# Optimization experiments

Hardware: AMD Instinct MI355X
Metric: run time of the kernel (lower is better)

Reference implementation:

```python
import jax, jax.numpy as jnp
import numpy as np
import math

D_MODEL = 512
HEADS = 8
D_K = D_MODEL // HEADS
N_CODES = 2048
BETA = 0.2
# conv stack config: (in_ch, out_ch, kernel, stride)
CONV_CFG = [(105, 64, 10, 3), (64, 128, 3, 2), (128, 256, 3, 2),
            (256, 512, 3, 2), (512, 512, 2, 2), (512, 512, 2, 2)]


def setup_inputs() -> dict:
    key = jax.random.key(0)
    ks = jax.random.split(key, 32)
    inp = {"x": jax.random.normal(ks[0], (64, 105, 5500), dtype=jnp.float32)}
    # conv weights [out, in, k] (OIW layout) + biases, scaled ~ 1/sqrt(fan_in)
    for i, (cin, cout, k, s) in enumerate(CONV_CFG):
        std = 1.0 / math.sqrt(cin * k)
        inp[f"w{i+1}"] = jax.random.normal(ks[1 + 2 * i], (cout, cin, k), dtype=jnp.float32) * std
        inp[f"b{i+1}"] = jax.random.normal(ks[2 + 2 * i], (cout,), dtype=jnp.float32) * std
    # per-head Q/K/V projections stacked: [H, D, d_k]
    std = 1.0 / math.sqrt(D_MODEL)
    inp["wq"] = jax.random.normal(ks[13], (HEADS, D_MODEL, D_K), dtype=jnp.float32) * std
    inp["wk"] = jax.random.normal(ks[14], (HEADS, D_MODEL, D_K), dtype=jnp.float32) * std
    inp["wv"] = jax.random.normal(ks[15], (HEADS, D_MODEL, D_K), dtype=jnp.float32) * std
    inp["wo"] = jax.random.normal(ks[16], (D_MODEL, D_MODEL), dtype=jnp.float32) * std
    inp["bo"] = jax.random.normal(ks[17], (D_MODEL,), dtype=jnp.float32) * std
    # codebook (nn.Embedding default init ~ N(0,1))
    inp["codebook"] = jax.random.normal(ks[18], (N_CODES, D_MODEL), dtype=jnp.float32)
    return inp


def _conv_stack(x, ws, bs):
    # x: [B, C, T]; valid 1D convs with given strides
    for w, b, (_, _, _, s) in zip(ws, bs, CONV_CFG):
        x = jax.lax.conv_general_dilated(
            x, w, window_strides=(s,), padding='VALID',
            dimension_numbers=('NCH', 'OIH', 'NCH'))
        x = x + b[None, :, None]
    return x  # [B, 512, 57]


def _mha(x, wq, wk, wv, wo, bo):
    # x: [B, L, D]
    q = jnp.einsum('bld,hdk->bhlk', x, wq)
    k = jnp.einsum('bld,hdk->bhlk', x, wk)
    v = jnp.einsum('bld,hdk->bhlk', x, wv)
    scores = jnp.einsum('bhlk,bhmk->bhlm', q, k) / math.sqrt(D_K)
    attn = jax.nn.softmax(scores, axis=-1)
    out = jnp.einsum('bhlm,bhmk->bhlk', attn, v)
    B, H, L, dk = out.shape
    out = out.transpose(0, 2, 1, 3).reshape(B, L, H * dk)  # concat heads
    return out @ wo + bo


def reference(x, w1, b1, w2, b2, w3, b3, w4, b4, w5, b5, w6, b6,
              wq, wk, wv, wo, bo, codebook):
    ws = [w1, w2, w3, w4, w5, w6]
    bs = [b1, b2, b3, b4, b5, b6]
    conv_out = _conv_stack(x, ws, bs).transpose(0, 2, 1)  # [B, 57, 512]
    attn = _mha(conv_out, wq, wk, wv, wo, bo)             # [B, 57, 512]
    # squared Euclidean distances to codebook (same argmin as cdist)
    d2 = (jnp.sum(attn * attn, axis=-1, keepdims=True)    # [B, L, 1]
          - 2.0 * jnp.einsum('bld,nd->bln', attn, codebook)
          + jnp.sum(codebook * codebook, axis=-1)[None, None, :])  # [B, L, N]
    indices = jnp.argmin(d2, axis=-1)                     # [B, L]
    z_q = codebook[indices]                               # [B, L, D]
    codebook_loss = jnp.mean((z_q - jax.lax.stop_gradient(attn)) ** 2)
    commitment_loss = jnp.mean((attn - jax.lax.stop_gradient(z_q)) ** 2)
    vq_loss = codebook_loss + BETA * commitment_loss
    z_q_st = attn + jax.lax.stop_gradient(z_q - attn)
    return z_q_st, vq_loss, indices
```

## Files before the change

kernel.cpp:

```cpp
#include <hip/hip_runtime.h>
#include <hip/hip_bf16.h>
#include <math.h>

#define B_ 64
#define HB_ 32
#define L_ 57
#define D_ 512
#define H_ 8
#define DK_ 64
#define NC_ 2048

__global__ __launch_bounds__(256) void wtrans_k(const float* __restrict__ w,
                                                float* __restrict__ wT,
                                                int CINK, int COUT)
{
  int idx = blockIdx.x * 256 + threadIdx.x;
  if (idx >= CINK * COUT) return;
  int r = idx / COUT, c = idx - r * COUT;
  wT[idx] = w[(size_t)c * CINK + r];
}

__global__ __launch_bounds__(256) void wqkvprep_k(
    const float* __restrict__ wq, const float* __restrict__ wk,
    const float* __restrict__ wv, float* __restrict__ wqkvT)
{
  int idx = blockIdx.x * 256 + threadIdx.x;
  if (idx >= 786432) return;
  int set = idx >> 18;
  int h   = (idx >> 15) & 7;
  int d   = (idx >> 6) & 511;
  int kd  = idx & 63;
  const float* W = (set == 0 ? wq : (set == 1 ? wk : wv));
  float v = W[((size_t)h * 512 + d) * 64 + kd];
  wqkvT[(size_t)d * 1536 + set * 512 + h * 64 + kd] = v;
}

template<int CIN, int K, int S, int COUT, int CC>
__global__ __launch_bounds__(256) void conv1d_k(
    const float* __restrict__ x, const float* __restrict__ wT,
    const float* __restrict__ bias, float* __restrict__ y,
    int Tin, int Tout)
{
  constexpr int TT = 64;
  constexpr int SPAN = S * TT + K - S;
  __shared__ float xs[CC * SPAN];
  const int b   = blockIdx.z;
  const int cbk = blockIdx.y;
  const int t0  = blockIdx.x * TT;
  const int tid = threadIdx.x;
  const int lane_t = tid & 63;
  const int g = tid >> 6;
  const int coutBase = __builtin_amdgcn_readfirstlane(cbk * 64 + g * 16);
  const int t = t0 + lane_t;
  float acc[16];
#pragma unroll
  for (int j = 0; j < 16; ++j) acc[j] = 0.f;
  const float* xb = x + (size_t)b * CIN * Tin;
  const int col0 = t0 * S;

  for (int c0 = 0; c0 < CIN; c0 += CC) {
    __syncthreads();
    for (int e = tid; e < CC * SPAN; e += 256) {
      int cc = e / SPAN, col = e - cc * SPAN;
      int ti = col0 + col;
      xs[e] = (ti < Tin) ? xb[(size_t)(c0 + cc) * Tin + ti] : 0.f;
    }
    __syncthreads();

    const float* wchunk = wT + ((size_t)c0 * K) * COUT + coutBase;
    for (int cc = 0; cc < CC; ++cc) {
#pragma unroll
      for (int kk = 0; kk < K; ++kk) {
        const float* wrow = wchunk + (size_t)(cc * K + kk) * COUT;
        float wv[16];
#pragma unroll
        for (int j = 0; j < 16; ++j) wv[j] = wrow[j];
        float xv = xs[cc * SPAN + lane_t * S + kk];
#pragma unroll
        for (int j = 0; j < 16; ++j) acc[j] += xv * wv[j];
      }
    }
  }
  if (t < Tout) {
#pragma unroll
    for (int j = 0; j < 16; ++j) {
      int co = coutBase + j;
      y[((size_t)b * COUT + co) * Tout + t] = acc[j] + bias[co];
    }
  }
}

template<int CINC, int K, int S, int COUT, int CC, int KS>
__global__ __launch_bounds__(256) void convks_k(
    const float* __restrict__ x, const float* __restrict__ wT,
    float* __restrict__ p, int Tin, int Tout, int bStrideX, int ksStrideP)
{
  constexpr int TT = 64;
  constexpr int SPAN = S * TT + K - S;
  __shared__ float xs[CC * SPAN];
  const int b   = blockIdx.z;
  const int cbk = blockIdx.y & 7;
  const int ks  = blockIdx.y >> 3;
  const int t0  = blockIdx.x * TT;
  const int tid = threadIdx.x;
  const int lane_t = tid & 63;
  const int g = tid >> 6;
  const int coutBase = __builtin_amdgcn_readfirstlane(cbk * 64 + g * 16);
  const int t = t0 + lane_t;
  float acc[16];
#pragma unroll
  for (int j = 0; j < 16; ++j) acc[j] = 0.f;
  const float* xb = x + (size_t)b * bStrideX + (size_t)ks * CINC * Tin;
  const float* wbase = wT + ((size_t)ks * CINC * K) * COUT;
  const int col0 = t0 * S;

  for (int c0 = 0; c0 < CINC; c0 += CC) {
    __syncthreads();
    for (int e = tid; e < CC * SPAN; e += 256) {
      int cc = e / SPAN, col = e - cc * SPAN;
      int ti = col0 + col;
      xs[e] = (ti < Tin) ? xb[(size_t)(c0 + cc) * Tin + ti] : 0.f;
    }
    __syncthreads();

    const float* wchunk = wbase + ((size_t)c0 * K) * COUT + coutBase;
    for (int cc = 0; cc < CC; ++cc) {
#pragma unroll
      for (int kk = 0; kk < K; ++kk) {
        const float* wrow = wchunk + (size_t)(cc * K + kk) * COUT;
        float wv[16];
#pragma unroll
        for (int j = 0; j < 16; ++j) wv[j] = wrow[j];
        float xv = xs[cc * SPAN + lane_t * S + kk];
#pragma unroll
        for (int j = 0; j < 16; ++j) acc[j] += xv * wv[j];
      }
    }
  }
  if (t < Tout) {
#pragma unroll
    for (int j = 0; j < 16; ++j) {
      int co = coutBase + j;
      p[(size_t)ks * ksStrideP + ((size_t)b * COUT + co) * Tout + t] = acc[j];
    }
  }
}

template<int COUT, int TOUT, int KS>
__global__ __launch_bounds__(256) void redbias_k(
    const float* __restrict__ p, const float* __restrict__ bias,
    float* __restrict__ y, int ksStride, int n)
{
  int idx = blockIdx.x * 256 + threadIdx.x;
  if (idx >= n) return;
  int c = (idx / TOUT) % COUT;
  float s = p[idx];
#pragma unroll
  for (int ks = 1; ks < KS; ++ks) s += p[idx + (size_t)ks * ksStride];
  y[idx] = s + bias[c];
}

__global__ __launch_bounds__(256) void itranspose_k(const float* __restrict__ y,
                                                    float* __restrict__ yT)
{
  const int b = blockIdx.y, dt = blockIdx.x;
  __shared__ float tile[32 * 58];
  const int tid = threadIdx.x;
  const int d0 = dt * 32;
  for (int e = tid; e < L_ * 32; e += 256) {
    int l = e >> 5, dd = e & 31;
    tile[dd * 58 + l] = y[((size_t)b * L_ + l) * D_ + d0 + dd];
  }
  __syncthreads();
  for (int e = tid; e < 32 * L_; e += 256) {
    int dd = e / L_, l = e - dd * L_;
    yT[((size_t)b * D_ + d0 + dd) * L_ + l] = tile[dd * 58 + l];
  }
}

__global__ __launch_bounds__(256, 2) void qkvgemm_k(
    const float* __restrict__ c6, const float* __restrict__ wqkvT,
    float* __restrict__ q, float* __restrict__ k, float* __restrict__ v)
{
  const int ot = blockIdx.x, b = blockIdx.y;
  const int tid = threadIdx.x;
  const int w = tid >> 6, lane = tid & 63;
  const int lrow = lane >> 3, ncol = lane & 7;
  __shared__ __align__(16) float As[32 * 68];
  __shared__ __align__(16) float Bs[32 * 256];
  float acc[8][8];
#pragma unroll
  for (int li = 0; li < 8; ++li)
#pragma unroll
    for (int nj = 0; nj < 8; ++nj) acc[li][nj] = 0.f;

  const float* c6b = c6 + (size_t)b * D_ * L_;
  const int o0 = ot * 256;

  for (int d0 = 0; d0 < D_; d0 += 32) {
    __syncthreads();
#pragma unroll
    for (int i = 0; i < 8; ++i) {
      int e = tid + i * 256;
      int dd = e >> 6, l = e & 63;
      As[dd * 68 + l] = (l < L_) ? c6b[(size_t)(d0 + dd) * L_ + l] : 0.f;
    }
#pragma unroll
    for (int i = 0; i < 8; ++i) {
      int e = tid + i * 256;
      int dd = e >> 6, o4 = (e & 63) * 4;
      *reinterpret_cast<float4*>(&Bs[dd * 256 + o4]) =
          *reinterpret_cast<const float4*>(&wqkvT[(size_t)(d0 + dd) * 1536 + o0 + o4]);
    }
    __syncthreads();
#pragma unroll 4
    for (int dd = 0; dd < 32; ++dd) {
      float a8[8], b8[8];
      *reinterpret_cast<float4*>(&a8[0]) = *reinterpret_cast<const float4*>(&As[dd * 68 + lrow * 8]);
      *reinterpret_cast<float4*>(&a8[4]) = *reinterpret_cast<const float4*>(&As[dd * 68 + lrow * 8 + 4]);
      *reinterpret_cast<float4*>(&b8[0]) = *reinterpret_cast<const float4*>(&Bs[dd * 256 + w * 64 + ncol * 8]);
      *reinterpret_cast<float4*>(&b8[4]) = *reinterpret_cast<const float4*>(&Bs[dd * 256 + w * 64 + ncol * 8 + 4]);
#pragma unroll
      for (int li = 0; li < 8; ++li)
#pragma unroll
        for (int nj = 0; nj < 8; ++nj)
          acc[li][nj] += a8[li] * b8[nj];
    }
  }

  const int o3 = o0 + w * 64 + ncol * 8;
  const int set = __builtin_amdgcn_readfirstlane(o3 >> 9);
  const int h = (o3 >> 6) & 7, kd = o3 & 63;
  float* OUT = (set == 0 ? q : (set == 1 ? k : v));
  float* base = OUT + (((size_t)b * H_ + h) * L_) * DK_ + kd;
#pragma unroll
  for (int li = 0; li < 8; ++li) {
    int l = lrow * 8 + li;
    if (l < L_) {
      float* p = base + (size_t)l * DK_;
      *reinterpret_cast<float4*>(p)     = *reinterpret_cast<float4*>(&acc[li][0]);
      *reinterpret_cast<float4*>(p + 4) = *reinterpret_cast<float4*>(&acc[li][4]);
    }
  }
}

__global__ __launch_bounds__(256) void attn_k(
    const float* __restrict__ q, const float* __restrict__ k, const float* __restrict__ v,
    float* __restrict__ cat)
{
  const int bh = blockIdx.x;
  const int b = bh >> 3, h = bh & 7;
  __shared__ float qs[L_ * DK_];
  __shared__ float ks[L_ * 65];
  __shared__ float vs[L_ * DK_];
  __shared__ float ps[L_ * DK_];
  const int tid = threadIdx.x;
  const float* qb = q + (size_t)bh * L_ * DK_;
  const float* kb = k + (size_t)bh * L_ * DK_;
  const float* vb = v + (size_t)bh * L_ * DK_;
  for (int e = tid; e < L_ * DK_; e += 256) {
    qs[e] = qb[e];
    vs[e] = vb[e];
    int m = e >> 6, d = e & 63;
    ks[m * 65 + d] = kb[e];
  }
  __syncthreads();
  for (int e = tid; e < L_ * L_; e += 256) {
    int l = e / L_, m = e - (e / L_) * L_;
    float s = 0.f;
#pragma unroll
    for (int d = 0; d < DK_; ++d) s += qs[l * DK_ + d] * ks[m * 65 + d];
    ps[l * DK_ + m] = s * 0.125f;
  }
  __syncthreads();
  if (tid < L_) {
    float mx = -1e30f;
    for (int m = 0; m < L_; ++m) mx = fmaxf(mx, ps[tid * DK_ + m]);
    float sum = 0.f;
    for (int m = 0; m < L_; ++m) { float e2 = __expf(ps[tid * DK_ + m] - mx); ps[tid * DK_ + m] = e2; sum += e2; }
    float inv = 1.f / sum;
    for (int m = 0; m < L_; ++m) ps[tid * DK_ + m] *= inv;
  }
  __syncthreads();
  for (int e = tid; e < L_ * DK_; e += 256) {
    int l = e >> 6, kd = e & 63;
    float s = 0.f;
    for (int m = 0; m < L_; ++m) s += ps[l * DK_ + m] * vs[m * DK_ + kd];
    cat[((size_t)b * L_ + l) * D_ + h * DK_ + kd] = s;
  }
}

__global__ __launch_bounds__(256) void outproj_k(
    const float* __restrict__ cat, const float* __restrict__ wo,
    const float* __restrict__ bo, float* __restrict__ y)
{
  const int b = blockIdx.y, lt = blockIdx.x;
  const int l0 = lt * 16;
  __shared__ __align__(16) float cs[16 * D_];
  const int tid = threadIdx.x;
  for (int e = tid; e < 16 * D_; e += 256) {
    int l = l0 + (e >> 9);
    cs[e] = (l < L_) ? cat[((size_t)b * L_ + l) * D_ + (e & 511)] : 0.f;
  }
  __syncthreads();
  float acc0[16], acc1[16];
#pragma unroll
  for (int j = 0; j < 16; ++j) { acc0[j] = 0.f; acc1[j] = 0.f; }
  for (int d = 0; d < D_; d += 4) {
    float w00 = wo[(size_t)d * D_ + tid];
    float w01 = wo[(size_t)(d + 1) * D_ + tid];
    float w02 = wo[(size_t)(d + 2) * D_ + tid];
    float w03 = wo[(size_t)(d + 3) * D_ + tid];
    float w10 = wo[(size_t)d * D_ + tid + 256];
    float w11 = wo[(size_t)(d + 1) * D_ + tid + 256];
    float w12 = wo[(size_t)(d + 2) * D_ + tid + 256];
    float w13 = wo[(size_t)(d + 3) * D_ + tid + 256];
#pragma unroll
    for (int j = 0; j < 16; ++j) {
      const float4 c4 = *reinterpret_cast<const float4*>(&cs[j * D_ + d]);
      acc0[j] += c4.x * w00 + c4.y * w01 + c4.z * w02 + c4.w * w03;
      acc1[j] += c4.x * w10 + c4.y * w11 + c4.z * w12 + c4.w * w13;
    }
  }
#pragma unroll
  for (int j = 0; j < 16; ++j) {
    int l = l0 + j;
    if (l < L_) {
      y[((size_t)b * L_ + l) * D_ + tid] = acc0[j] + bo[tid];
      y[((size_t)b * L_ + l) * D_ + tid + 256] = acc1[j] + bo[tid + 256];
    }
  }
}

__global__ __launch_bounds__(64) void cbprep_k(const float* __restrict__ cb,
                                               float* __restrict__ cbT,
                                               float* __restrict__ cnorm)
{
  const int n = blockIdx.x, t = threadIdx.x;
  float s = 0.f;
  for (int d = t; d < D_; d += 64) {
    float vv = cb[(size_t)n * D_ + d];
    cbT[(size_t)d * NC_ + n] = vv;
    s += vv * vv;
  }
#pragma unroll
  for (int off = 32; off >= 1; off >>= 1) s += __shfl_xor(s, off);
  if (t == 0) cnorm[n] = s;
}

__global__ __launch_bounds__(256, 2) void vqgemm_k(
    const float* __restrict__ yT, const float* __restrict__ cbT,
    const float* __restrict__ cnorm, float* __restrict__ pmin, int* __restrict__ pidx)
{
  const int b = blockIdx.y, nt = blockIdx.x;
  const int tid = threadIdx.x;
  const int w = tid >> 6, lane = tid & 63;
  const int lrow = lane >> 3, ncol = lane & 7;
  __shared__ __align__(16) float As[32 * 68];
  __shared__ __align__(16) float Bs[32 * 256];
  __shared__ float redv[4][64];
  __shared__ int   redi[4][64];
  float acc[8][8];
#pragma unroll
  for (int li = 0; li < 8; ++li)
#pragma unroll
    for (int nj = 0; nj < 8; ++nj) acc[li][nj] = 0.f;

  const float* yTb = yT + (size_t)b * D_ * L_;
  const int n0 = nt * 256;
  const int nbase = n0 + w * 64 + ncol * 8;

  for (int d0 = 0; d0 < D_; d0 += 32) {
    __syncthreads();
#pragma unroll
    for (int i = 0; i < 8; ++i) {
      int e = tid + i * 256;
      int dd = e >> 6, l = e & 63;
      As[dd * 68 + l] = (l < L_) ? yTb[(size_t)(d0 + dd) * L_ + l] : 0.f;
    }
#pragma unroll
    for (int i = 0; i < 8; ++i) {
      int e = tid + i * 256;
      int dd = e >> 6, n4 = (e & 63) * 4;
      *reinterpret_cast<float4*>(&Bs[dd * 256 + n4]) =
          *reinterpret_cast<const float4*>(&cbT[(size_t)(d0 + dd) * NC_ + n0 + n4]);
    }
    __syncthreads();
#pragma unroll 4
    for (int dd = 0; dd < 32; ++dd) {
      float a8[8], b8[8];
      *reinterpret_cast<float4*>(&a8[0]) = *reinterpret_cast<const float4*>(&As[dd * 68 + lrow * 8]);
      *reinterpret_cast<float4*>(&a8[4]) = *reinterpret_cast<const float4*>(&As[dd * 68 + lrow * 8 + 4]);
      *reinterpret_cast<float4*>(&b8[0]) = *reinterpret_cast<const float4*>(&Bs[dd * 256 + w * 64 + ncol * 8]);
      *reinterpret_cast<float4*>(&b8[4]) = *reinterpret_cast<const float4*>(&Bs[dd * 256 + w * 64 + ncol * 8 + 4]);
#pragma unroll
      for (int li = 0; li < 8; ++li)
#pragma unroll
        for (int nj = 0; nj < 8; ++nj)
          acc[li][nj] += a8[li] * b8[nj];
    }
  }

  float cn[8];
  *reinterpret_cast<float4*>(&cn[0]) = *reinterpret_cast<const float4*>(&cnorm[nbase]);
  *reinterpret_cast<float4*>(&cn[4]) = *reinterpret_cast<const float4*>(&cnorm[nbase + 4]);
#pragma unroll
  for (int li = 0; li < 8; ++li) {
    float vb = cn[0] - 2.f * acc[li][0];
    int ib = nbase;
#pragma unroll
    for (int nj = 1; nj < 8; ++nj) {
      float v = cn[nj] - 2.f * acc[li][nj];
      if (v < vb) { vb = v; ib = nbase + nj; }
    }
#pragma unroll
    for (int off = 1; off <= 4; off <<= 1) {
      float vo = __shfl_xor(vb, off);
      int io = __shfl_xor(ib, off);
      if (vo < vb || (vo == vb && io < ib)) { vb = vo; ib = io; }
    }
    if (ncol == 0) { redv[w][lrow * 8 + li] = vb; redi[w][lrow * 8 + li] = ib; }
  }
  __syncthreads();
  if (tid < L_) {
    float vb = redv[0][tid]; int ib = redi[0][tid];
#pragma unroll
    for (int w2 = 1; w2 < 4; ++w2) {
      float vo = redv[w2][tid]; int io = redi[w2][tid];
      if (vo < vb || (vo == vb && io < ib)) { vb = vo; ib = io; }
    }
    pmin[((size_t)b * L_ + tid) * 8 + nt] = vb;
    pidx[((size_t)b * L_ + tid) * 8 + nt] = ib;
  }
}

__global__ __launch_bounds__(64) void vqfin_k(
    const float* __restrict__ y, const float* __restrict__ cbook,
    const float* __restrict__ pmin, const int* __restrict__ pidx,
    float* __restrict__ zq, float* __restrict__ oidx, float* __restrict__ lpart)
{
  const int bl = blockIdx.x;
  const int tid = threadIdx.x;
  __shared__ int sidx;
  if (tid == 0) {
    float vb = pmin[(size_t)bl * 8];
    int ib = pidx[(size_t)bl * 8];
    for (int ntv = 1; ntv < 8; ++ntv) {
      float vo = pmin[(size_t)bl * 8 + ntv];
      int io = pidx[(size_t)bl * 8 + ntv];
      if (vo < vb || (vo == vb && io < ib)) { vb = vo; ib = io; }
    }
    sidx = ib;
  }
  __syncthreads();
  const int idx = sidx;
  const float* crow = cbook + (size_t)idx * D_;
  const float* yrow = y + (size_t)bl * D_;
  float s = 0.f;
  for (int d = tid; d < D_; d += 64) {
    float c = crow[d];
    float df = c - yrow[d];
    zq[(size_t)bl * D_ + d] = c;
    s += df * df;
  }
#pragma unroll
  for (int off = 32; off >= 1; off >>= 1) s += __shfl_xor(s, off);
  if (tid == 0) { lpart[bl] = s; oidx[bl] = (float)idx; }
}

__global__ __launch_bounds__(256) void loss_k(const float* __restrict__ lpart,
                                              float* __restrict__ outLoss)
{
  const int tid = threadIdx.x;
  float s = 0.f;
  for (int i = tid; i < B_ * L_; i += 256) s += lpart[i];
  __shared__ float red[256];
  red[tid] = s;
  __syncthreads();
  for (int off = 128; off >= 1; off >>= 1) {
    if (tid < off) red[tid] += red[tid + off];
    __syncthreads();
  }
  if (tid == 0) outLoss[0] = red[0] * ((1.f + 0.2f) / (float)((size_t)B_ * L_ * D_));
}

extern "C" void kernel_launch(void* const* d_in, const int* in_sizes, int n_in,
                              void* d_out, int out_size, void* d_ws, size_t ws_size,
                              hipStream_t stream)
{
  const float* x  = (const float*)d_in[0];
  const float* w1 = (const float*)d_in[1];  const float* b1 = (const float*)d_in[2];
  const float* w2 = (const float*)d_in[3];  const float* b2 = (const float*)d_in[4];
  const float* w3 = (const float*)d_in[5];  const float* b3 = (const float*)d_in[6];
  const float* w4 = (const float*)d_in[7];  const float* b4 = (const float*)d_in[8];
  const float* w5 = (const float*)d_in[9];  const float* b5 = (const float*)d_in[10];
  const float* w6 = (const float*)d_in[11]; const float* b6 = (const float*)d_in[12];
  const float* wq = (const float*)d_in[13];
  const float* wk = (const float*)d_in[14];
  const float* wv = (const float*)d_in[15];
  const float* wo = (const float*)d_in[16];
  const float* bo = (const float*)d_in[17];
  const float* cbook = (const float*)d_in[18];

  float* ws = (float*)d_ws;
  float* wT1 = ws;
  float* wT2 = ws + 67200;
  float* wT3 = ws + 91776;
  float* wT4 = ws + 190080;
  float* wT5 = ws + 583296;
  float* wT6 = ws + 1107584;
  float* bufA = ws + 1632000;
  float* bufB = ws + 5382016;
  float* c6   = ws + 9132032;
  float* qb     = ws;
  float* kb     = ws + 1867776;
  float* vb     = ws + 3735552;
  float* wqkvT  = ws + 5603328;
  float* cat    = ws + 7471104;
  float* yattn  = ws + 9338880;
  float* cbT    = ws + 11206656;
  float* cnorm  = ws + 12255232;
  float* pminb  = ws + 12257280;
  int*   pidxb  = (int*)(ws + 12286464);
  float* lpart  = ws + 12315648;
  float* yT     = ws;

  float* zq      = (float*)d_out;
  float* outLoss = zq + (size_t)B_ * L_ * D_;
  float* outIdx  = outLoss + 1;

  wtrans_k<<<(1050 * 64 + 255) / 256, 256, 0, stream>>>(w1, wT1, 1050, 64);
  wtrans_k<<<( 192 * 128 + 255) / 256, 256, 0, stream>>>(w2, wT2, 192, 128);
  wtrans_k<<<( 384 * 256 + 255) / 256, 256, 0, stream>>>(w3, wT3, 384, 256);
  wtrans_k<<<( 768 * 512 + 255) / 256, 256, 0, stream>>>(w4, wT4, 768, 512);
  wtrans_k<<<(1024 * 512 + 255) / 256, 256, 0, stream>>>(w5, wT5, 1024, 512);
  wtrans_k<<<(1024 * 512 + 255) / 256, 256, 0, stream>>>(w6, wT6, 1024, 512);

  for (int h = 0; h < 2; ++h) {
    const float* xh = x + (size_t)h * HB_ * 105 * 5500;
    float* c6h = c6 + (size_t)h * HB_ * D_ * L_;
    conv1d_k<105,10,3, 64,35><<<dim3(29,1,HB_),256,0,stream>>>(xh,   wT1,b1, bufA, 5500,1831);
    conv1d_k< 64, 3,2,128,64><<<dim3(15,2,HB_),256,0,stream>>>(bufA, wT2,b2, bufB, 1831, 915);
    conv1d_k<128, 3,2,256,64><<<dim3( 8,4,HB_),256,0,stream>>>(bufB, wT3,b3, bufA,  915, 457);
    conv1d_k<256, 3,2,512,64><<<dim3( 4,8,HB_),256,0,stream>>>(bufA, wT4,b4, bufB,  457, 228);
    convks_k<256,2,2,512,64,2><<<dim3(2,16,HB_),256,0,stream>>>(
        bufB, wT5, bufA, 228, 114, 512 * 228, 1867776);
    redbias_k<512,114,2><<<(1867776 + 255) / 256, 256, 0, stream>>>(
        bufA, b5, bufB, 1867776, 1867776);
    convks_k<128,2,2,512,64,4><<<dim3(1,32,HB_),256,0,stream>>>(
        bufB, wT6, bufA, 114, 57, 512 * 114, 933888);
    redbias_k<512,57,4><<<(933888 + 255) / 256, 256, 0, stream>>>(
        bufA, b6, c6h, 933888, 933888);
  }

  wqkvprep_k<<<(786432 + 255) / 256, 256, 0, stream>>>(wq, wk, wv, wqkvT);
  qkvgemm_k<<<dim3(6, B_), 256, 0, stream>>>(c6, wqkvT, qb, kb, vb);
  cbprep_k<<<NC_, 64, 0, stream>>>(cbook, cbT, cnorm);
  attn_k<<<B_ * H_, 256, 0, stream>>>(qb, kb, vb, cat);
  outproj_k<<<dim3(4, B_), 256, 0, stream>>>(cat, wo, bo, yattn);

  itranspose_k<<<dim3(16, B_), 256, 0, stream>>>(yattn, yT);
  vqgemm_k<<<dim3(8, B_), 256, 0, stream>>>(yT, cbT, cnorm, pminb, pidxb);
  vqfin_k<<<B_ * L_, 64, 0, stream>>>(yattn, cbook, pminb, pidxb, zq, outIdx, lpart);
  loss_k<<<1, 256, 0, stream>>>(lpart, outLoss);
}
```

Before: 1.379 ms.

## Unify conv kernels with channel-interleaved LDS layout and split-K first conv

Merges the two conv kernels into one templated kernel. It stores the input tile in shared memory as [time][channel] with padding, so each thread reads two channels at once with a float2 load. The first conv layer is now split across two channel groups, with weights zero-padded to a multiple of the chunk size, and a reduction-plus-bias pass afterwards. This gives the largest layer more blocks and cuts LDS load instructions. The cost is an extra partial-sum write and read for layer 1, plus more weight-row loads held in registers at the same time.

```diff
diff --git a/kernel.cpp b/kernel.cpp
--- a/kernel.cpp
+++ b/kernel.cpp
@@ -10,14 +10,14 @@
 #define DK_ 64
 #define NC_ 2048
 
-__global__ __launch_bounds__(256) void wtrans_k(const float* __restrict__ w,
-                                                float* __restrict__ wT,
-                                                int CINK, int COUT)
+__global__ __launch_bounds__(256) void wtransp_k(const float* __restrict__ w,
+                                                 float* __restrict__ wT,
+                                                 int CINK, int CINK_PAD, int COUT)
 {
   int idx = blockIdx.x * 256 + threadIdx.x;
-  if (idx >= CINK * COUT) return;
+  if (idx >= CINK_PAD * COUT) return;
   int r = idx / COUT, c = idx - r * COUT;
-  wT[idx] = w[(size_t)c * CINK + r];
+  wT[idx] = (r < CINK) ? w[(size_t)c * CINK + r] : 0.f;
 }
 
 __global__ __launch_bounds__(256) void wqkvprep_k(
@@ -35,17 +35,21 @@
   wqkvT[(size_t)d * 1536 + set * 512 + h * 64 + kd] = v;
 }
 
-template<int CIN, int K, int S, int COUT, int CC>
-__global__ __launch_bounds__(256) void conv1d_k(
+template<int CC, int K, int S, int COUT, bool PARTIAL>
+__global__ __launch_bounds__(256) void convq_k(
     const float* __restrict__ x, const float* __restrict__ wT,
     const float* __restrict__ bias, float* __restrict__ y,
-    int Tin, int Tout)
+    int Tin, int Tout, int CINtot, int nChunks, int nCoutBlk,
+    int ksStrideP, int cinPerKs)
 {
   constexpr int TT = 64;
   constexpr int SPAN = S * TT + K - S;
-  __shared__ float xs[CC * SPAN];
+  constexpr int CCP = CC + 2;
+  __shared__ __align__(16) float xs[SPAN * CCP];
   const int b   = blockIdx.z;
-  const int cbk = blockIdx.y;
+  const int yb  = blockIdx.y;
+  const int cbk = yb % nCoutBlk;
+  const int ks  = yb / nCoutBlk;
   const int t0  = blockIdx.x * TT;
   const int tid = threadIdx.x;
   const int lane_t = tid & 63;
@@ -55,29 +59,39 @@
   float acc[16];
 #pragma unroll
   for (int j = 0; j < 16; ++j) acc[j] = 0.f;
-  const float* xb = x + (size_t)b * CIN * Tin;
+  const float* xb = x + (size_t)b * CINtot * Tin;
   const int col0 = t0 * S;
-
-  for (int c0 = 0; c0 < CIN; c0 += CC) {
+  const int cinBase = ks * cinPerKs;
+
+  for (int ch = 0; ch < nChunks; ++ch) {
+    const int cin0 = cinBase + ch * CC;
     __syncthreads();
     for (int e = tid; e < CC * SPAN; e += 256) {
       int cc = e / SPAN, col = e - cc * SPAN;
+      int gci = cin0 + cc;
       int ti = col0 + col;
-      xs[e] = (ti < Tin) ? xb[(size_t)(c0 + cc) * Tin + ti] : 0.f;
-    }
-    __syncthreads();
-
-    const float* wchunk = wT + ((size_t)c0 * K) * COUT + coutBase;
-    for (int cc = 0; cc < CC; ++cc) {
+      float v = 0.f;
+      if (ti < Tin && gci < CINtot) v = xb[(size_t)gci * Tin + ti];
+      xs[col * CCP + cc] = v;
+    }
+    __syncthreads();
+
+    const float* wch = wT + ((size_t)cin0 * K) * COUT + coutBase;
+    for (int cp = 0; cp < CC / 2; ++cp) {
 #pragma unroll
       for (int kk = 0; kk < K; ++kk) {
-        const float* wrow = wchunk + (size_t)(cc * K + kk) * COUT;
-        float wv[16];
-#pragma unroll
-        for (int j = 0; j < 16; ++j) wv[j] = wrow[j];
-        float xv = xs[cc * SPAN + lane_t * S + kk];
-#pragma unroll
-        for (int j = 0; j < 16; ++j) acc[j] += xv * wv[j];
+        const float2 xv = *reinterpret_cast<const float2*>(
+            &xs[(lane_t * S + kk) * CCP + cp * 2]);
+        const float* w0 = wch + (size_t)((cp * 2) * K + kk) * COUT;
+        const float* w1 = wch + (size_t)((cp * 2 + 1) * K + kk) * COUT;
+        float wv0[16], wv1[16];
+#pragma unroll
+        for (int j = 0; j < 16; ++j) wv0[j] = w0[j];
+#pragma unroll
+        for (int j = 0; j < 16; ++j) wv1[j] = w1[j];
+#pragma unroll
+        for (int j = 0; j < 16; ++j)
+          acc[j] += xv.x * wv0[j] + xv.y * wv1[j];
       }
     }
   }
@@ -85,63 +99,11 @@
 #pragma unroll
     for (int j = 0; j < 16; ++j) {
       int co = coutBase + j;
-      y[((size_t)b * COUT + co) * Tout + t] = acc[j] + bias[co];
-    }
-  }
-}
-
-template<int CINC, int K, int S, int COUT, int CC, int KS>
-__global__ __launch_bounds__(256) void convks_k(
-    const float* __restrict__ x, const float* __restrict__ wT,
-    float* __restrict__ p, int Tin, int Tout, int bStrideX, int ksStrideP)
-{
-  constexpr int TT = 64;
-  constexpr int SPAN = S * TT + K - S;
-  __shared__ float xs[CC * SPAN];
-  const int b   = blockIdx.z;
-  const int cbk = blockIdx.y & 7;
-  const int ks  = blockIdx.y >> 3;
-  const int t0  = blockIdx.x * TT;
-  const int tid = threadIdx.x;
-  const int lane_t = tid & 63;
-  const int g = tid >> 6;
-  const int coutBase = __builtin_amdgcn_readfirstlane(cbk * 64 + g * 16);
-  const int t = t0 + lane_t;
-  float acc[16];
-#pragma unroll
-  for (int j = 0; j < 16; ++j) acc[j] = 0.f;
-  const float* xb = x + (size_t)b * bStrideX + (size_t)ks * CINC * Tin;
-  const float* wbase = wT + ((size_t)ks * CINC * K) * COUT;
-  const int col0 = t0 * S;
-
-  for (int c0 = 0; c0 < CINC; c0 += CC) {
-    __syncthreads();
-    for (int e = tid; e < CC * SPAN; e += 256) {
-      int cc = e / SPAN, col = e - cc * SPAN;
-      int ti = col0 + col;
-      xs[e] = (ti < Tin) ? xb[(size_t)(c0 + cc) * Tin + ti] : 0.f;
-    }
-    __syncthreads();
-
-    const float* wchunk = wbase + ((size_t)c0 * K) * COUT + coutBase;
-    for (int cc = 0; cc < CC; ++cc) {
-#pragma unroll
-      for (int kk = 0; kk < K; ++kk) {
-        const float* wrow = wchunk + (size_t)(cc * K + kk) * COUT;
-        float wv[16];
-#pragma unroll
-        for (int j = 0; j < 16; ++j) wv[j] = wrow[j];
-        float xv = xs[cc * SPAN + lane_t * S + kk];
-#pragma unroll
-        for (int j = 0; j < 16; ++j) acc[j] += xv * wv[j];
+      if (PARTIAL) {
+        y[(size_t)ks * ksStrideP + ((size_t)b * COUT + co) * Tout + t] = acc[j];
+      } else {
+        y[((size_t)b * COUT + co) * Tout + t] = acc[j] + bias[co];
       }
-    }
-  }
-  if (t < Tout) {
-#pragma unroll
-    for (int j = 0; j < 16; ++j) {
-      int co = coutBase + j;
-      p[(size_t)ks * ksStrideP + ((size_t)b * COUT + co) * Tout + t] = acc[j];
     }
   }
 }
@@ -504,51 +466,57 @@
 
   float* ws = (float*)d_ws;
   float* wT1 = ws;
-  float* wT2 = ws + 67200;
-  float* wT3 = ws + 91776;
-  float* wT4 = ws + 190080;
-  float* wT5 = ws + 583296;
-  float* wT6 = ws + 1107584;
-  float* bufA = ws + 1632000;
-  float* bufB = ws + 5382016;
-  float* c6   = ws + 9132032;
+  float* wT2 = ws + 71680;
+  float* wT3 = ws + 96256;
+  float* wT4 = ws + 194560;
+  float* wT5 = ws + 587776;
+  float* wT6 = ws + 1112064;
+  float* bufA = ws + 1640000;
+  float* bufB = ws + 5390016;
+  float* c6   = ws + 9140032;
   float* qb     = ws;
   float* kb     = ws + 1867776;
   float* vb     = ws + 3735552;
   float* wqkvT  = ws + 5603328;
   float* cat    = ws + 7471104;
-  float* yattn  = ws + 9338880;
+  float* yattn  = ws;
+  float* yT     = ws + 1867776;
   float* cbT    = ws + 11206656;
   float* cnorm  = ws + 12255232;
   float* pminb  = ws + 12257280;
   int*   pidxb  = (int*)(ws + 12286464);
   float* lpart  = ws + 12315648;
-  float* yT     = ws;
 
   float* zq      = (float*)d_out;
   float* outLoss = zq + (size_t)B_ * L_ * D_;
   float* outIdx  = outLoss + 1;
 
-  wtrans_k<<<(1050 * 64 + 255) / 256, 256, 0, stream>>>(w1, wT1, 1050, 64);
-  wtrans_k<<<( 192 * 128 + 255) / 256, 256, 0, stream>>>(w2, wT2, 192, 128);
-  wtrans_k<<<( 384 * 256 + 255) / 256, 256, 0, stream>>>(w3, wT3, 384, 256);
-  wtrans_k<<<( 768 * 512 + 255) / 256, 256, 0, stream>>>(w4, wT4, 768, 512);
-  wtrans_k<<<(1024 * 512 + 255) / 256, 256, 0, stream>>>(w5, wT5, 1024, 512);
-  wtrans_k<<<(1024 * 512 + 255) / 256, 256, 0, stream>>>(w6, wT6, 1024, 512);
+  wtransp_k<<<(1120 * 64 + 255) / 256, 256, 0, stream>>>(w1, wT1, 1050, 1120, 64);
+  wtransp_k<<<( 192 * 128 + 255) / 256, 256, 0, stream>>>(w2, wT2, 192, 192, 128);
+  wtransp_k<<<( 384 * 256 + 255) / 256, 256, 0, stream>>>(w3, wT3, 384, 384, 256);
+  wtransp_k<<<( 768 * 512 + 255) / 256, 256, 0, stream>>>(w4, wT4, 768, 768, 512);
+  wtransp_k<<<(1024 * 512 + 255) / 256, 256, 0, stream>>>(w5, wT5, 1024, 1024, 512);
+  wtransp_k<<<(1024 * 512 + 255) / 256, 256, 0, stream>>>(w6, wT6, 1024, 1024, 512);
 
   for (int h = 0; h < 2; ++h) {
     const float* xh = x + (size_t)h * HB_ * 105 * 5500;
     float* c6h = c6 + (size_t)h * HB_ * D_ * L_;
-    conv1d_k<105,10,3, 64,35><<<dim3(29,1,HB_),256,0,stream>>>(xh,   wT1,b1, bufA, 5500,1831);
-    conv1d_k< 64, 3,2,128,64><<<dim3(15,2,HB_),256,0,stream>>>(bufA, wT2,b2, bufB, 1831, 915);
-    conv1d_k<128, 3,2,256,64><<<dim3( 8,4,HB_),256,0,stream>>>(bufB, wT3,b3, bufA,  915, 457);
-    conv1d_k<256, 3,2,512,64><<<dim3( 4,8,HB_),256,0,stream>>>(bufA, wT4,b4, bufB,  457, 228);
-    convks_k<256,2,2,512,64,2><<<dim3(2,16,HB_),256,0,stream>>>(
-        bufB, wT5, bufA, 228, 114, 512 * 228, 1867776);
+    convq_k<28,10,3, 64,true ><<<dim3(29, 2,HB_),256,0,stream>>>(
+        xh, wT1, b1, bufA, 5500, 1831, 105, 2, 1, 3750016, 56);
+    redbias_k<64,1831,2><<<(3749888 + 255) / 256, 256, 0, stream>>>(
+        bufA, b1, bufA, 3750016, 3749888);
+    convq_k<32, 3,2,128,false><<<dim3(15, 2,HB_),256,0,stream>>>(
+        bufA, wT2, b2, bufB, 1831, 915, 64, 2, 2, 0, 0);
+    convq_k<32, 3,2,256,false><<<dim3( 8, 4,HB_),256,0,stream>>>(
+        bufB, wT3, b3, bufA, 915, 457, 128, 4, 4, 0, 0);
+    convq_k<32, 3,2,512,false><<<dim3( 4, 8,HB_),256,0,stream>>>(
+        bufA, wT4, b4, bufB, 457, 228, 256, 8, 8, 0, 0);
+    convq_k<32, 2,2,512,true ><<<dim3( 2,16,HB_),256,0,stream>>>(
+        bufB, wT5, b5, bufA, 228, 114, 512, 8, 8, 1867776, 256);
     redbias_k<512,114,2><<<(1867776 + 255) / 256, 256, 0, stream>>>(
         bufA, b5, bufB, 1867776, 1867776);
-    convks_k<128,2,2,512,64,4><<<dim3(1,32,HB_),256,0,stream>>>(
-        bufB, wT6, bufA, 114, 57, 512 * 114, 933888);
+    convq_k<32, 2,2,512,true ><<<dim3( 1,32,HB_),256,0,stream>>>(
+        bufB, wT6, b6, bufA, 114, 57, 512, 4, 8, 933888, 128);
     redbias_k<512,57,4><<<(933888 + 255) / 256, 256, 0, stream>>>(
         bufA, b6, c6h, 933888, 933888);
   }
```

New measurement: 2.275 ms. 65.0% more time.
